# Performance work log

Measured on AMD Instinct MI355X. Metric: run time of the kernel, lower is better.

Reference implementation:

```python
import jax, jax.numpy as jnp
import numpy as np

ALPHA = 0.2  # leaky-relu negative slope
N_NODES = 50000
IN_F = 256
OUT_F = 64
N_EDGES = 1600000


def setup_inputs() -> dict:
    key = jax.random.key(0)
    k1, k2, k3, k4 = jax.random.split(key, 4)
    x = jax.random.normal(k1, (N_NODES, IN_F), dtype=jnp.float32)
    # xavier_normal-ish scales for params
    W = jax.random.normal(k2, (IN_F, OUT_F), dtype=jnp.float32) * (1.414 * (2.0 / (IN_F + OUT_F)) ** 0.5)
    a = jax.random.normal(k3, (1, 2 * OUT_F), dtype=jnp.float32) * (1.414 * (2.0 / (1 + 2 * OUT_F)) ** 0.5)
    edge_index = jax.random.randint(k4, (2, N_EDGES), 0, N_NODES, dtype=jnp.int64)
    return {"x": x, "W": W, "a": a, "edge_index": edge_index}


def reference(x, W, a, edge_index):
    N = x.shape[0]
    src = edge_index[0]  # row index of sparse adjacency (aggregation target)
    dst = edge_index[1]  # column index (neighbor being gathered)
    h = x @ W  # [N, out]
    out_f = h.shape[1]
    # a @ cat(h[src], h[dst]) == (h @ a1)[src] + (h @ a2)[dst]
    a1 = a[0, :out_f]
    a2 = a[0, out_f:]
    s_src = h @ a1  # [N]
    s_dst = h @ a2  # [N]
    score = s_src[src] + s_dst[dst]  # [E]
    edge_e = jnp.exp(-jax.nn.leaky_relu(score, negative_slope=ALPHA))  # [E]
    # e_rowsum[i] = sum_{e: src==i} edge_e[e]
    e_rowsum = jax.ops.segment_sum(edge_e, src, num_segments=N)  # [N]
    # h_prime[i] = sum_{e: src==i} edge_e[e] * h[dst[e]]
    h_prime = jax.ops.segment_sum(edge_e[:, None] * h[dst], src, num_segments=N)  # [N, out]
    h_prime = h_prime / e_rowsum[:, None]
    return jax.nn.elu(h_prime)
```

## Files before the change

kernel.cpp:

```cpp
#include <hip/hip_runtime.h>
#include <hip/hip_bf16.h>


#define ALPHA 0.2f
#define KDIM 256
#define FDIM 64

typedef __bf16 bf16x8 __attribute__((ext_vector_type(8)));
typedef float f32x4 __attribute__((ext_vector_type(4)));
typedef unsigned int u32;
typedef unsigned short u16;

#define BIN_CHUNK 8192
#define BUCKET_CAP 16384

__global__ __launch_bounds__(256) void gat_wt_kernel(
    const float* __restrict__ W, __hip_bfloat16* __restrict__ w_t)
{
    const int t = blockIdx.x * 256 + threadIdx.x;
    if (t < KDIM * FDIM) {
        const int k = t >> 6;
        const int n = t & 63;
        w_t[n * KDIM + k] = __float2bfloat16(W[t]);
    }
}

__global__ __launch_bounds__(256) void gat_gemm_kernel(
    const float* __restrict__ x, const __hip_bfloat16* __restrict__ w_tp,
    const float* __restrict__ a, __hip_bfloat16* __restrict__ h_bf,
    float* __restrict__ s_src, float* __restrict__ s_dst, int N)
{
    const int lane = threadIdx.x & 63;
    const int wv = threadIdx.x >> 6;
    const int m0 = blockIdx.x * 64 + wv * 16;
    const int c = lane & 15;
    const int q = lane >> 4;

    const int mrow = m0 + c;
    const float* xp = x + (long)(mrow < N ? mrow : N - 1) * KDIM;
    const __bf16* wt = (const __bf16*)w_tp;

    f32x4 acc[4];
#pragma unroll
    for (int ct = 0; ct < 4; ++ct) acc[ct] = (f32x4){0.f, 0.f, 0.f, 0.f};

#pragma unroll 2
    for (int kc = 0; kc < 8; ++kc) {
        const int k0 = kc * 32 + q * 8;
        const float4 xa = *(const float4*)(xp + k0);
        const float4 xb = *(const float4*)(xp + k0 + 4);
        bf16x8 af;
        af[0] = (__bf16)xa.x; af[1] = (__bf16)xa.y;
        af[2] = (__bf16)xa.z; af[3] = (__bf16)xa.w;
        af[4] = (__bf16)xb.x; af[5] = (__bf16)xb.y;
        af[6] = (__bf16)xb.z; af[7] = (__bf16)xb.w;
#pragma unroll
        for (int ct = 0; ct < 4; ++ct) {
            const bf16x8 bf = *(const bf16x8*)(wt + (ct * 16 + c) * KDIM + k0);
            acc[ct] = __builtin_amdgcn_mfma_f32_16x16x32_bf16(af, bf, acc[ct], 0, 0, 0);
        }
    }

    float a1c[4], a2c[4];
#pragma unroll
    for (int ct = 0; ct < 4; ++ct) {
        a1c[ct] = a[ct * 16 + c];
        a2c[ct] = a[FDIM + ct * 16 + c];
    }
    float s1r[4], s2r[4];
#pragma unroll
    for (int reg = 0; reg < 4; ++reg) {
        float s1 = 0.f, s2 = 0.f;
#pragma unroll
        for (int ct = 0; ct < 4; ++ct) {
            s1 += acc[ct][reg] * a1c[ct];
            s2 += acc[ct][reg] * a2c[ct];
        }
        s1r[reg] = s1; s2r[reg] = s2;
    }
#pragma unroll
    for (int off = 1; off < 16; off <<= 1) {
#pragma unroll
        for (int reg = 0; reg < 4; ++reg) {
            s1r[reg] += __shfl_xor(s1r[reg], off);
            s2r[reg] += __shfl_xor(s2r[reg], off);
        }
    }

#pragma unroll
    for (int reg = 0; reg < 4; ++reg) {
        const int row = m0 + q * 4 + reg;
        if (row < N) {
#pragma unroll
            for (int ct = 0; ct < 4; ++ct)
                h_bf[(long)row * FDIM + ct * 16 + c] = __float2bfloat16(acc[ct][reg]);
            if (c == 0) { s_src[row] = s1r[reg]; s_dst[row] = s2r[reg]; }
        }
    }
}

__global__ __launch_bounds__(256) void gat_bhist_kernel(
    const int* __restrict__ srcA, int* __restrict__ bcnt, int E, int NB)
{
    __shared__ int hist[256];
    const int t = threadIdx.x;
    hist[t] = 0;
    __syncthreads();
    const int base = blockIdx.x * BIN_CHUNK;
    const int cnt = min(BIN_CHUNK, E - base);
    for (int i = t; i < cnt; i += 256)
        atomicAdd(&hist[srcA[base + i] >> 8], 1);
    __syncthreads();
    if (t < NB && hist[t] > 0) atomicAdd(&bcnt[t], hist[t]);
}

__global__ __launch_bounds__(256) void gat_bscan_kernel(
    const int* __restrict__ bcnt, int* __restrict__ bbase,
    int* __restrict__ bcur, int NB)
{
    __shared__ int wsum[4];
    const int t = threadIdx.x;
    const int lane = t & 63;
    const int w = t >> 6;
    const int v = (t < NB) ? bcnt[t] : 0;
    int incl = v;
#pragma unroll
    for (int off = 1; off < 64; off <<= 1) {
        const int nv = __shfl_up(incl, off);
        if (lane >= off) incl += nv;
    }
    if (lane == 63) wsum[w] = incl;
    __syncthreads();
    int woff = 0;
    if (w > 0) woff += wsum[0];
    if (w > 1) woff += wsum[1];
    if (w > 2) woff += wsum[2];
    const int excl = woff + incl - v;
    bbase[t] = excl;
    if (t < NB) bcur[t] = excl;
    if (t == 0) bbase[256] = wsum[0] + wsum[1] + wsum[2] + wsum[3];
}

__global__ __launch_bounds__(256) void gat_bin_kernel(
    const int* __restrict__ srcA, const int* __restrict__ dstA,
    int* __restrict__ bcur, u32* __restrict__ pair, int E, int NB)
{
    __shared__ u32 chunk[BIN_CHUNK];
    __shared__ int hist[256];
    __shared__ int lcur[256];
    const int t = threadIdx.x;
    hist[t] = 0;
    __syncthreads();

    const int base = blockIdx.x * BIN_CHUNK;
    const int cnt = min(BIN_CHUNK, E - base);
    for (int i = t; i < cnt; i += 256) {
        const int s = srcA[base + i];
        const int d = dstA[base + i];
        chunk[i] = ((u32)(s >> 8) << 24) | ((u32)(s & 255) << 16) | (u32)d;
        atomicAdd(&hist[s >> 8], 1);
    }
    __syncthreads();
    if (t < NB) lcur[t] = (hist[t] > 0) ? atomicAdd(&bcur[t], hist[t]) : 0;
    __syncthreads();
    for (int i = t; i < cnt; i += 256) {
        const u32 p = chunk[i];
        const int b = p >> 24;
        const int pos = atomicAdd(&lcur[b], 1);
        pair[pos] = p & 0x00FFFFFFu;
    }
}

__global__ __launch_bounds__(256) void gat_bsort_kernel(
    const u32* __restrict__ pair, const int* __restrict__ bbase,
    int* __restrict__ offs, int* __restrict__ sorted_dst, int N, int NB)
{
    __shared__ u32 chunk[BUCKET_CAP];
    __shared__ u16 sorted_l[BUCKET_CAP];
    __shared__ int cur[256];
    __shared__ int wsum[4];

    const int b = blockIdx.x;
    const int t = threadIdx.x;
    const int lane = t & 63;
    const int w = t >> 6;
    const int s0 = b << 8;
    const int e0 = bbase[b];
    const int e1 = bbase[b + 1];
    const int n = min(e1 - e0, BUCKET_CAP);

    cur[t] = 0;
    __syncthreads();
    for (int i = t; i < n; i += 256) {
        const u32 p = pair[e0 + i];
        chunk[i] = p;
        atomicAdd(&cur[p >> 16], 1);
    }
    __syncthreads();
    const int v = cur[t];
    int incl = v;
#pragma unroll
    for (int off = 1; off < 64; off <<= 1) {
        const int nv = __shfl_up(incl, off);
        if (lane >= off) incl += nv;
    }
    if (lane == 63) wsum[w] = incl;
    __syncthreads();
    int woff = 0;
    if (w > 0) woff += wsum[0];
    if (w > 1) woff += wsum[1];
    if (w > 2) woff += wsum[2];
    const int excl = woff + incl - v;
    if (s0 + t < N) offs[s0 + t] = e0 + excl;
    if (b == NB - 1 && t == 0) offs[N] = e1;
    __syncthreads();
    cur[t] = excl;
    __syncthreads();
    for (int i = t; i < n; i += 256) {
        const u32 p = chunk[i];
        const int slot = atomicAdd(&cur[p >> 16], 1);
        sorted_l[slot] = (u16)(p & 0xFFFFu);
    }
    __syncthreads();
    for (int i = t; i < n; i += 256)
        sorted_dst[e0 + i] = (int)sorted_l[i];
}

__global__ __launch_bounds__(256) void gat_gather_kernel(
    const int* __restrict__ offs, const int* __restrict__ sorted_dst,
    const float* __restrict__ s_src, const float* __restrict__ s_dst,
    const __hip_bfloat16* __restrict__ h_bf, float* __restrict__ out, int N)
{
    const int node = blockIdx.x * 4 + (threadIdx.x >> 6);
    if (node >= N) return;
    const int lane = threadIdx.x & 63;
    const int q = lane >> 3;
    const int c = lane & 7;

    const int start = offs[node];
    const int end = offs[node + 1];
    const float ssrc = s_src[node];
    const __bf16* hb = (const __bf16*)h_bf;

    float acc[8];
#pragma unroll
    for (int j = 0; j < 8; ++j) acc[j] = 0.f;
    float wsum = 0.f;

    for (int e = start + q; e < end; e += 8) {
        const int d = sorted_dst[e];
        const float sc = ssrc + s_dst[d];
        const float lr = sc > 0.f ? sc : ALPHA * sc;
        const float wgt = __expf(-lr);
        const bf16x8 hv = *(const bf16x8*)(hb + (long)d * FDIM + 8 * c);
#pragma unroll
        for (int j = 0; j < 8; ++j) acc[j] += wgt * (float)hv[j];
        wsum += wgt;
    }

#pragma unroll
    for (int off = 8; off < 64; off <<= 1) {
#pragma unroll
        for (int j = 0; j < 8; ++j) acc[j] += __shfl_xor(acc[j], off);
        wsum += __shfl_xor(wsum, off);
    }

    if (q == 0) {
        const float inv = 1.0f / wsum;
        float o[8];
#pragma unroll
        for (int j = 0; j < 8; ++j) {
            const float v = acc[j] * inv;
            o[j] = v > 0.f ? v : expm1f(v);
        }
        float* op = &out[(long)node * FDIM + 8 * c];
        *(float4*)op = make_float4(o[0], o[1], o[2], o[3]);
        *(float4*)(op + 4) = make_float4(o[4], o[5], o[6], o[7]);
    }
}

extern "C" void kernel_launch(void* const* d_in, const int* in_sizes, int n_in,
                              void* d_out, int out_size, void* d_ws, size_t ws_size,
                              hipStream_t stream) {
    const float* x = (const float*)d_in[0];
    const float* W = (const float*)d_in[1];
    const float* a = (const float*)d_in[2];
    const int* ei  = (const int*)d_in[3];

    const int N = in_sizes[0] / KDIM;
    const int E = in_sizes[3] / 2;
    const int NB = (N + 255) >> 8;
    const int* srcA = ei;
    const int* dstA = ei + E;

    __hip_bfloat16* h_bf = (__hip_bfloat16*)d_ws;
    __hip_bfloat16* w_t  = h_bf + (size_t)N * FDIM;
    float* s_src = (float*)(w_t + KDIM * FDIM);
    float* s_dst = s_src + N;
    int* offs    = (int*)(s_dst + N);
    int* bcnt    = offs + N + 4;
    int* bbase   = bcnt + 256;
    int* bcur    = bbase + 260;
    u32* pair    = (u32*)(bcur + 256);
    int* sorted_dst = (int*)(pair + E);
    float* out   = (float*)d_out;

    hipMemsetAsync(bcnt, 0, 256 * sizeof(int), stream);

    gat_wt_kernel<<<dim3((KDIM * FDIM + 255) / 256), dim3(256), 0, stream>>>(W, w_t);
    gat_gemm_kernel<<<dim3((N + 63) / 64), dim3(256), 0, stream>>>(
        x, w_t, a, h_bf, s_src, s_dst, N);

    const int nchunks = (E + BIN_CHUNK - 1) / BIN_CHUNK;
    gat_bhist_kernel<<<dim3(nchunks), dim3(256), 0, stream>>>(srcA, bcnt, E, NB);
    gat_bscan_kernel<<<dim3(1), dim3(256), 0, stream>>>(bcnt, bbase, bcur, NB);
    gat_bin_kernel<<<dim3(nchunks), dim3(256), 0, stream>>>(srcA, dstA, bcur, pair, E, NB);
    gat_bsort_kernel<<<dim3(NB), dim3(256), 0, stream>>>(pair, bbase, offs, sorted_dst, N, NB);

    gat_gather_kernel<<<dim3((N + 3) / 4), dim3(256), 0, stream>>>(
        offs, sorted_dst, s_src, s_dst, h_bf, out, N);
}
```

Baseline: 205.0 us.

## Restructure edge binning into per-chunk local sort and precompute fp16 edge weights

Replaces the global histogram, scan and atomic binning pipeline with a per-chunk local counting sort that records per-chunk bucket offsets. A single-block kernel then derives bucket bases, and the bucket sort gathers its segments from every chunk. The bucket sort also computes each edge's attention weight and packs it as fp16 into the high half of the destination index, so the gather kernel no longer reads s_src/s_dst or evaluates exp. This removes the memset, one kernel and the global atomics. In exchange, every bucket block walks all chunk offset tables, weights lose precision in fp16, and the 16-bit dst packing assumes N < 65536.

```diff
diff --git a/kernel.cpp b/kernel.cpp
--- a/kernel.cpp
+++ b/kernel.cpp
@@ -1,18 +1,19 @@
 #include <hip/hip_runtime.h>
 #include <hip/hip_bf16.h>
+#include <hip/hip_fp16.h>
 
 
 #define ALPHA 0.2f
 #define KDIM 256
 #define FDIM 64
+#define BIN_CHUNK 8192
+#define BUCKET_CAP 16384
+#define OFFW 257
 
 typedef __bf16 bf16x8 __attribute__((ext_vector_type(8)));
 typedef float f32x4 __attribute__((ext_vector_type(4)));
 typedef unsigned int u32;
 typedef unsigned short u16;
-
-#define BIN_CHUNK 8192
-#define BUCKET_CAP 16384
 
 __global__ __launch_bounds__(256) void gat_wt_kernel(
     const float* __restrict__ W, __hip_bfloat16* __restrict__ w_t)
@@ -99,30 +100,25 @@
     }
 }
 
-__global__ __launch_bounds__(256) void gat_bhist_kernel(
-    const int* __restrict__ srcA, int* __restrict__ bcnt, int E, int NB)
+__global__ __launch_bounds__(256) void gat_bin_kernel(
+    const int* __restrict__ srcA, const int* __restrict__ dstA,
+    int* __restrict__ off_blk, u32* __restrict__ pair, int E)
 {
     __shared__ int hist[256];
-    const int t = threadIdx.x;
-    hist[t] = 0;
-    __syncthreads();
-    const int base = blockIdx.x * BIN_CHUNK;
-    const int cnt = min(BIN_CHUNK, E - base);
-    for (int i = t; i < cnt; i += 256)
-        atomicAdd(&hist[srcA[base + i] >> 8], 1);
-    __syncthreads();
-    if (t < NB && hist[t] > 0) atomicAdd(&bcnt[t], hist[t]);
-}
-
-__global__ __launch_bounds__(256) void gat_bscan_kernel(
-    const int* __restrict__ bcnt, int* __restrict__ bbase,
-    int* __restrict__ bcur, int NB)
-{
+    __shared__ int cur[256];
     __shared__ int wsum[4];
     const int t = threadIdx.x;
     const int lane = t & 63;
     const int w = t >> 6;
-    const int v = (t < NB) ? bcnt[t] : 0;
+    const int base = blockIdx.x * BIN_CHUNK;
+    const int cnt = min(BIN_CHUNK, E - base);
+
+    hist[t] = 0;
+    __syncthreads();
+    for (int i = t; i < cnt; i += 256) atomicAdd(&hist[srcA[base + i] >> 8], 1);
+    __syncthreads();
+
+    const int v = hist[t];
     int incl = v;
 #pragma unroll
     for (int off = 1; off < 64; off <<= 1) {
@@ -136,67 +132,85 @@
     if (w > 1) woff += wsum[1];
     if (w > 2) woff += wsum[2];
     const int excl = woff + incl - v;
-    bbase[t] = excl;
-    if (t < NB) bcur[t] = excl;
-    if (t == 0) bbase[256] = wsum[0] + wsum[1] + wsum[2] + wsum[3];
-}
-
-__global__ __launch_bounds__(256) void gat_bin_kernel(
-    const int* __restrict__ srcA, const int* __restrict__ dstA,
-    int* __restrict__ bcur, u32* __restrict__ pair, int E, int NB)
-{
-    __shared__ u32 chunk[BIN_CHUNK];
-    __shared__ int hist[256];
-    __shared__ int lcur[256];
-    const int t = threadIdx.x;
-    hist[t] = 0;
-    __syncthreads();
-
-    const int base = blockIdx.x * BIN_CHUNK;
-    const int cnt = min(BIN_CHUNK, E - base);
+    off_blk[blockIdx.x * OFFW + t] = excl;
+    if (t == 0) off_blk[blockIdx.x * OFFW + 256] = cnt;
+    cur[t] = excl;
+    __syncthreads();
+
     for (int i = t; i < cnt; i += 256) {
         const int s = srcA[base + i];
         const int d = dstA[base + i];
-        chunk[i] = ((u32)(s >> 8) << 24) | ((u32)(s & 255) << 16) | (u32)d;
-        atomicAdd(&hist[s >> 8], 1);
-    }
-    __syncthreads();
-    if (t < NB) lcur[t] = (hist[t] > 0) ? atomicAdd(&bcur[t], hist[t]) : 0;
-    __syncthreads();
-    for (int i = t; i < cnt; i += 256) {
-        const u32 p = chunk[i];
-        const int b = p >> 24;
-        const int pos = atomicAdd(&lcur[b], 1);
-        pair[pos] = p & 0x00FFFFFFu;
-    }
+        const int pos = atomicAdd(&cur[s >> 8], 1);
+        pair[base + pos] = ((u32)(s & 255) << 16) | (u32)d;
+    }
+}
+
+__global__ __launch_bounds__(256) void gat_bbase_kernel(
+    const int* __restrict__ off_blk, int* __restrict__ bbase, int NBLK)
+{
+    __shared__ int wsum[4];
+    const int t = threadIdx.x;
+    const int lane = t & 63;
+    const int w = t >> 6;
+    int total = 0;
+    for (int blk = 0; blk < NBLK; ++blk) {
+        const int* ob = off_blk + blk * OFFW;
+        total += ob[t + 1] - ob[t];
+    }
+    int incl = total;
+#pragma unroll
+    for (int off = 1; off < 64; off <<= 1) {
+        const int nv = __shfl_up(incl, off);
+        if (lane >= off) incl += nv;
+    }
+    if (lane == 63) wsum[w] = incl;
+    __syncthreads();
+    int woff = 0;
+    if (w > 0) woff += wsum[0];
+    if (w > 1) woff += wsum[1];
+    if (w > 2) woff += wsum[2];
+    const int excl = woff + incl - total;
+    bbase[t] = excl;
+    if (t == 255) bbase[256] = excl + total;
 }
 
 __global__ __launch_bounds__(256) void gat_bsort_kernel(
-    const u32* __restrict__ pair, const int* __restrict__ bbase,
-    int* __restrict__ offs, int* __restrict__ sorted_dst, int N, int NB)
+    const u32* __restrict__ pair, const int* __restrict__ off_blk,
+    const int* __restrict__ bbase, const float* __restrict__ s_src,
+    const float* __restrict__ s_dst, int* __restrict__ offs,
+    u32* __restrict__ sorted_pk, int N, int NBLK, int NB)
 {
     __shared__ u32 chunk[BUCKET_CAP];
-    __shared__ u16 sorted_l[BUCKET_CAP];
     __shared__ int cur[256];
+    __shared__ float ssl[256];
     __shared__ int wsum[4];
 
     const int b = blockIdx.x;
     const int t = threadIdx.x;
     const int lane = t & 63;
     const int w = t >> 6;
-    const int s0 = b << 8;
     const int e0 = bbase[b];
     const int e1 = bbase[b + 1];
     const int n = min(e1 - e0, BUCKET_CAP);
 
+    int pos = 0;
+    for (int blk = 0; blk < NBLK; ++blk) {
+        const int s = off_blk[blk * OFFW + b];
+        const int c = off_blk[blk * OFFW + b + 1] - s;
+        const u32* pp = pair + blk * BIN_CHUNK + s;
+        for (int i = t; i < c; i += 256) {
+            const int dp = pos + i;
+            if (dp < BUCKET_CAP) chunk[dp] = pp[i];
+        }
+        pos += c;
+    }
     cur[t] = 0;
-    __syncthreads();
-    for (int i = t; i < n; i += 256) {
-        const u32 p = pair[e0 + i];
-        chunk[i] = p;
-        atomicAdd(&cur[p >> 16], 1);
-    }
-    __syncthreads();
+    ssl[t] = (b * 256 + t < N) ? s_src[b * 256 + t] : 0.f;
+    __syncthreads();
+
+    for (int i = t; i < n; i += 256) atomicAdd(&cur[chunk[i] >> 16], 1);
+    __syncthreads();
+
     const int v = cur[t];
     int incl = v;
 #pragma unroll
@@ -211,24 +225,27 @@
     if (w > 1) woff += wsum[1];
     if (w > 2) woff += wsum[2];
     const int excl = woff + incl - v;
-    if (s0 + t < N) offs[s0 + t] = e0 + excl;
+    if (b * 256 + t < N) offs[b * 256 + t] = e0 + excl;
     if (b == NB - 1 && t == 0) offs[N] = e1;
     __syncthreads();
     cur[t] = excl;
     __syncthreads();
+
     for (int i = t; i < n; i += 256) {
         const u32 p = chunk[i];
-        const int slot = atomicAdd(&cur[p >> 16], 1);
-        sorted_l[slot] = (u16)(p & 0xFFFFu);
-    }
-    __syncthreads();
-    for (int i = t; i < n; i += 256)
-        sorted_dst[e0 + i] = (int)sorted_l[i];
+        const int sl = p >> 16;
+        const int d = (int)(p & 0xFFFFu);
+        const int slot = atomicAdd(&cur[sl], 1);
+        const float sc = ssl[sl] + s_dst[d];
+        const float lr = sc > 0.f ? sc : ALPHA * sc;
+        const float wgt = __expf(-lr);
+        const u32 wh = (u32)__half_as_ushort(__float2half(wgt));
+        sorted_pk[e0 + slot] = (u32)d | (wh << 16);
+    }
 }
 
 __global__ __launch_bounds__(256) void gat_gather_kernel(
-    const int* __restrict__ offs, const int* __restrict__ sorted_dst,
-    const float* __restrict__ s_src, const float* __restrict__ s_dst,
+    const int* __restrict__ offs, const u32* __restrict__ sorted_pk,
     const __hip_bfloat16* __restrict__ h_bf, float* __restrict__ out, int N)
 {
     const int node = blockIdx.x * 4 + (threadIdx.x >> 6);
@@ -239,7 +256,6 @@
 
     const int start = offs[node];
     const int end = offs[node + 1];
-    const float ssrc = s_src[node];
     const __bf16* hb = (const __bf16*)h_bf;
 
     float acc[8];
@@ -247,11 +263,11 @@
     for (int j = 0; j < 8; ++j) acc[j] = 0.f;
     float wsum = 0.f;
 
+#pragma unroll 2
     for (int e = start + q; e < end; e += 8) {
-        const int d = sorted_dst[e];
-        const float sc = ssrc + s_dst[d];
-        const float lr = sc > 0.f ? sc : ALPHA * sc;
-        const float wgt = __expf(-lr);
+        const u32 p = sorted_pk[e];
+        const float wgt = __half2float(__ushort_as_half((u16)(p >> 16)));
+        const int d = (int)(p & 0xFFFFu);
         const bf16x8 hv = *(const bf16x8*)(hb + (long)d * FDIM + 8 * c);
 #pragma unroll
         for (int j = 0; j < 8; ++j) acc[j] += wgt * (float)hv[j];
@@ -290,6 +306,7 @@
     const int N = in_sizes[0] / KDIM;
     const int E = in_sizes[3] / 2;
     const int NB = (N + 255) >> 8;
+    const int NBLK = (E + BIN_CHUNK - 1) / BIN_CHUNK;
     const int* srcA = ei;
     const int* dstA = ei + E;
 
@@ -298,25 +315,21 @@
     float* s_src = (float*)(w_t + KDIM * FDIM);
     float* s_dst = s_src + N;
     int* offs    = (int*)(s_dst + N);
-    int* bcnt    = offs + N + 4;
-    int* bbase   = bcnt + 256;
-    int* bcur    = bbase + 260;
-    u32* pair    = (u32*)(bcur + 256);
-    int* sorted_dst = (int*)(pair + E);
+    int* off_blk = offs + N + 4;
+    int* bbase   = off_blk + NBLK * OFFW;
+    u32* pair    = (u32*)(bbase + 260);
+    u32* sorted_pk = pair + E;
     float* out   = (float*)d_out;
-
-    hipMemsetAsync(bcnt, 0, 256 * sizeof(int), stream);
 
     gat_wt_kernel<<<dim3((KDIM * FDIM + 255) / 256), dim3(256), 0, stream>>>(W, w_t);
     gat_gemm_kernel<<<dim3((N + 63) / 64), dim3(256), 0, stream>>>(
         x, w_t, a, h_bf, s_src, s_dst, N);
 
-    const int nchunks = (E + BIN_CHUNK - 1) / BIN_CHUNK;
-    gat_bhist_kernel<<<dim3(nchunks), dim3(256), 0, stream>>>(srcA, bcnt, E, NB);
-    gat_bscan_kernel<<<dim3(1), dim3(256), 0, stream>>>(bcnt, bbase, bcur, NB);
-    gat_bin_kernel<<<dim3(nchunks), dim3(256), 0, stream>>>(srcA, dstA, bcur, pair, E, NB);
-    gat_bsort_kernel<<<dim3(NB), dim3(256), 0, stream>>>(pair, bbase, offs, sorted_dst, N, NB);
+    gat_bin_kernel<<<dim3(NBLK), dim3(256), 0, stream>>>(srcA, dstA, off_blk, pair, E);
+    gat_bbase_kernel<<<dim3(1), dim3(256), 0, stream>>>(off_blk, bbase, NBLK);
+    gat_bsort_kernel<<<dim3(NB), dim3(256), 0, stream>>>(
+        pair, off_blk, bbase, s_src, s_dst, offs, sorted_pk, N, NBLK, NB);
 
     gat_gather_kernel<<<dim3((N + 3) / 4), dim3(256), 0, stream>>>(
-        offs, sorted_dst, s_src, s_dst, h_bf, out, N);
-}
+        offs, sorted_pk, h_bf, out, N);
+}
```

Result: slower. 293.0 us (+42.9%).

## Use finer 64-node buckets and precompute fp16 edge weights during bucket sort

Applied to the files above, without the earlier changes.

Buckets shrink from 256 to 64 source nodes, which gives 782 sort blocks and smaller shared arrays. The bin kernel now re-reads src/dst instead of staging them in shared memory. The sort kernel computes each edge's attention weight and packs it as fp16 with the 16-bit dst index, so the gather no longer does the random s_dst lookup or the exp. This adds fp16 rounding of the weights, relies on dst fitting in 16 bits and bucket counts fitting BUCKET_CAP, and adds an unroll hint to the gather loop.

```diff
diff --git a/kernel.cpp b/kernel.cpp
--- a/kernel.cpp
+++ b/kernel.cpp
@@ -1,18 +1,18 @@
 #include <hip/hip_runtime.h>
 #include <hip/hip_bf16.h>
+#include <hip/hip_fp16.h>
 
 
 #define ALPHA 0.2f
 #define KDIM 256
 #define FDIM 64
+#define BIN_CHUNK 8192
+#define BUCKET_CAP 4096
 
 typedef __bf16 bf16x8 __attribute__((ext_vector_type(8)));
 typedef float f32x4 __attribute__((ext_vector_type(4)));
 typedef unsigned int u32;
 typedef unsigned short u16;
-
-#define BIN_CHUNK 8192
-#define BUCKET_CAP 16384
 
 __global__ __launch_bounds__(256) void gat_wt_kernel(
     const float* __restrict__ W, __hip_bfloat16* __restrict__ w_t)
@@ -100,30 +100,33 @@
 }
 
 __global__ __launch_bounds__(256) void gat_bhist_kernel(
-    const int* __restrict__ srcA, int* __restrict__ bcnt, int E, int NB)
-{
-    __shared__ int hist[256];
+    const int* __restrict__ srcA, int* __restrict__ bcnt, int E, int NBU)
+{
+    __shared__ int hist[1024];
     const int t = threadIdx.x;
-    hist[t] = 0;
+    for (int j = t; j < 1024; j += 256) hist[j] = 0;
     __syncthreads();
     const int base = blockIdx.x * BIN_CHUNK;
     const int cnt = min(BIN_CHUNK, E - base);
     for (int i = t; i < cnt; i += 256)
-        atomicAdd(&hist[srcA[base + i] >> 8], 1);
-    __syncthreads();
-    if (t < NB && hist[t] > 0) atomicAdd(&bcnt[t], hist[t]);
+        atomicAdd(&hist[srcA[base + i] >> 6], 1);
+    __syncthreads();
+    for (int j = t; j < NBU; j += 256) {
+        const int v = hist[j];
+        if (v) atomicAdd(&bcnt[j], v);
+    }
 }
 
 __global__ __launch_bounds__(256) void gat_bscan_kernel(
-    const int* __restrict__ bcnt, int* __restrict__ bbase,
-    int* __restrict__ bcur, int NB)
+    const int* __restrict__ bcnt, int* __restrict__ bbase, int* __restrict__ bcur)
 {
     __shared__ int wsum[4];
     const int t = threadIdx.x;
     const int lane = t & 63;
     const int w = t >> 6;
-    const int v = (t < NB) ? bcnt[t] : 0;
-    int incl = v;
+    const int4 v = *(const int4*)&bcnt[4 * t];
+    const int tsum = v.x + v.y + v.z + v.w;
+    int incl = tsum;
 #pragma unroll
     for (int off = 1; off < 64; off <<= 1) {
         const int nv = __shfl_up(incl, off);
@@ -135,61 +138,60 @@
     if (w > 0) woff += wsum[0];
     if (w > 1) woff += wsum[1];
     if (w > 2) woff += wsum[2];
-    const int excl = woff + incl - v;
-    bbase[t] = excl;
-    if (t < NB) bcur[t] = excl;
-    if (t == 0) bbase[256] = wsum[0] + wsum[1] + wsum[2] + wsum[3];
+    const int e0 = woff + incl - tsum;
+    const int4 o = make_int4(e0, e0 + v.x, e0 + v.x + v.y, e0 + v.x + v.y + v.z);
+    *(int4*)&bbase[4 * t] = o;
+    *(int4*)&bcur[4 * t] = o;
+    if (t == 255) bbase[1024] = e0 + tsum;
 }
 
 __global__ __launch_bounds__(256) void gat_bin_kernel(
     const int* __restrict__ srcA, const int* __restrict__ dstA,
-    int* __restrict__ bcur, u32* __restrict__ pair, int E, int NB)
-{
-    __shared__ u32 chunk[BIN_CHUNK];
-    __shared__ int hist[256];
-    __shared__ int lcur[256];
+    int* __restrict__ bcur, u32* __restrict__ pair, int E, int NBU)
+{
+    __shared__ int hist[1024];
+    __shared__ int lcur[1024];
     const int t = threadIdx.x;
-    hist[t] = 0;
-    __syncthreads();
-
+    for (int j = t; j < 1024; j += 256) hist[j] = 0;
+    __syncthreads();
     const int base = blockIdx.x * BIN_CHUNK;
     const int cnt = min(BIN_CHUNK, E - base);
+    for (int i = t; i < cnt; i += 256)
+        atomicAdd(&hist[srcA[base + i] >> 6], 1);
+    __syncthreads();
+    for (int j = t; j < NBU; j += 256) {
+        const int v = hist[j];
+        lcur[j] = v ? atomicAdd(&bcur[j], v) : 0;
+    }
+    __syncthreads();
     for (int i = t; i < cnt; i += 256) {
         const int s = srcA[base + i];
         const int d = dstA[base + i];
-        chunk[i] = ((u32)(s >> 8) << 24) | ((u32)(s & 255) << 16) | (u32)d;
-        atomicAdd(&hist[s >> 8], 1);
-    }
-    __syncthreads();
-    if (t < NB) lcur[t] = (hist[t] > 0) ? atomicAdd(&bcur[t], hist[t]) : 0;
-    __syncthreads();
-    for (int i = t; i < cnt; i += 256) {
-        const u32 p = chunk[i];
-        const int b = p >> 24;
-        const int pos = atomicAdd(&lcur[b], 1);
-        pair[pos] = p & 0x00FFFFFFu;
+        const int pos = atomicAdd(&lcur[s >> 6], 1);
+        pair[pos] = ((u32)(s & 63) << 16) | (u32)d;
     }
 }
 
 __global__ __launch_bounds__(256) void gat_bsort_kernel(
     const u32* __restrict__ pair, const int* __restrict__ bbase,
-    int* __restrict__ offs, int* __restrict__ sorted_dst, int N, int NB)
+    const float* __restrict__ s_src, const float* __restrict__ s_dst,
+    int* __restrict__ offs, u32* __restrict__ sorted_pk, int N, int NBU)
 {
     __shared__ u32 chunk[BUCKET_CAP];
-    __shared__ u16 sorted_l[BUCKET_CAP];
-    __shared__ int cur[256];
-    __shared__ int wsum[4];
+    __shared__ int cur[64];
+    __shared__ float ssl[64];
 
     const int b = blockIdx.x;
     const int t = threadIdx.x;
-    const int lane = t & 63;
-    const int w = t >> 6;
-    const int s0 = b << 8;
+    const int s0 = b << 6;
     const int e0 = bbase[b];
     const int e1 = bbase[b + 1];
     const int n = min(e1 - e0, BUCKET_CAP);
 
-    cur[t] = 0;
+    if (t < 64) {
+        cur[t] = 0;
+        ssl[t] = (s0 + t < N) ? s_src[s0 + t] : 0.f;
+    }
     __syncthreads();
     for (int i = t; i < n; i += 256) {
         const u32 p = pair[e0 + i];
@@ -197,38 +199,35 @@
         atomicAdd(&cur[p >> 16], 1);
     }
     __syncthreads();
-    const int v = cur[t];
-    int incl = v;
-#pragma unroll
-    for (int off = 1; off < 64; off <<= 1) {
-        const int nv = __shfl_up(incl, off);
-        if (lane >= off) incl += nv;
-    }
-    if (lane == 63) wsum[w] = incl;
-    __syncthreads();
-    int woff = 0;
-    if (w > 0) woff += wsum[0];
-    if (w > 1) woff += wsum[1];
-    if (w > 2) woff += wsum[2];
-    const int excl = woff + incl - v;
-    if (s0 + t < N) offs[s0 + t] = e0 + excl;
-    if (b == NB - 1 && t == 0) offs[N] = e1;
-    __syncthreads();
-    cur[t] = excl;
+    if (t < 64) {
+        const int v = cur[t];
+        int incl = v;
+#pragma unroll
+        for (int off = 1; off < 64; off <<= 1) {
+            const int nv = __shfl_up(incl, off);
+            if (t >= off) incl += nv;
+        }
+        const int excl = incl - v;
+        if (s0 + t < N) offs[s0 + t] = e0 + excl;
+        cur[t] = excl;
+    }
+    if (b == NBU - 1 && t == 0) offs[N] = e1;
     __syncthreads();
     for (int i = t; i < n; i += 256) {
         const u32 p = chunk[i];
-        const int slot = atomicAdd(&cur[p >> 16], 1);
-        sorted_l[slot] = (u16)(p & 0xFFFFu);
-    }
-    __syncthreads();
-    for (int i = t; i < n; i += 256)
-        sorted_dst[e0 + i] = (int)sorted_l[i];
+        const int sl = p >> 16;
+        const int d = (int)(p & 0xFFFFu);
+        const int slot = atomicAdd(&cur[sl], 1);
+        const float sc = ssl[sl] + s_dst[d];
+        const float lr = sc > 0.f ? sc : ALPHA * sc;
+        const float wgt = __expf(-lr);
+        const u32 wh = (u32)__half_as_ushort(__float2half(wgt));
+        sorted_pk[e0 + slot] = (u32)d | (wh << 16);
+    }
 }
 
 __global__ __launch_bounds__(256) void gat_gather_kernel(
-    const int* __restrict__ offs, const int* __restrict__ sorted_dst,
-    const float* __restrict__ s_src, const float* __restrict__ s_dst,
+    const int* __restrict__ offs, const u32* __restrict__ sorted_pk,
     const __hip_bfloat16* __restrict__ h_bf, float* __restrict__ out, int N)
 {
     const int node = blockIdx.x * 4 + (threadIdx.x >> 6);
@@ -239,7 +238,6 @@
 
     const int start = offs[node];
     const int end = offs[node + 1];
-    const float ssrc = s_src[node];
     const __bf16* hb = (const __bf16*)h_bf;
 
     float acc[8];
@@ -247,11 +245,11 @@
     for (int j = 0; j < 8; ++j) acc[j] = 0.f;
     float wsum = 0.f;
 
+#pragma unroll 2
     for (int e = start + q; e < end; e += 8) {
-        const int d = sorted_dst[e];
-        const float sc = ssrc + s_dst[d];
-        const float lr = sc > 0.f ? sc : ALPHA * sc;
-        const float wgt = __expf(-lr);
+        const u32 p = sorted_pk[e];
+        const float wgt = __half2float(__ushort_as_half((u16)(p >> 16)));
+        const int d = (int)(p & 0xFFFFu);
         const bf16x8 hv = *(const bf16x8*)(hb + (long)d * FDIM + 8 * c);
 #pragma unroll
         for (int j = 0; j < 8; ++j) acc[j] += wgt * (float)hv[j];
@@ -289,7 +287,8 @@
 
     const int N = in_sizes[0] / KDIM;
     const int E = in_sizes[3] / 2;
-    const int NB = (N + 255) >> 8;
+    const int NBU = (N + 63) >> 6;
+    const int NBLK = (E + BIN_CHUNK - 1) / BIN_CHUNK;
     const int* srcA = ei;
     const int* dstA = ei + E;
 
@@ -299,24 +298,24 @@
     float* s_dst = s_src + N;
     int* offs    = (int*)(s_dst + N);
     int* bcnt    = offs + N + 4;
-    int* bbase   = bcnt + 256;
-    int* bcur    = bbase + 260;
-    u32* pair    = (u32*)(bcur + 256);
-    int* sorted_dst = (int*)(pair + E);
+    int* bbase   = bcnt + 1024;
+    int* bcur    = bbase + 1028;
+    u32* pair    = (u32*)(bcur + 1024);
+    u32* sorted_pk = pair + E;
     float* out   = (float*)d_out;
 
-    hipMemsetAsync(bcnt, 0, 256 * sizeof(int), stream);
+    hipMemsetAsync(bcnt, 0, 1024 * sizeof(int), stream);
 
     gat_wt_kernel<<<dim3((KDIM * FDIM + 255) / 256), dim3(256), 0, stream>>>(W, w_t);
     gat_gemm_kernel<<<dim3((N + 63) / 64), dim3(256), 0, stream>>>(
         x, w_t, a, h_bf, s_src, s_dst, N);
 
-    const int nchunks = (E + BIN_CHUNK - 1) / BIN_CHUNK;
-    gat_bhist_kernel<<<dim3(nchunks), dim3(256), 0, stream>>>(srcA, bcnt, E, NB);
-    gat_bscan_kernel<<<dim3(1), dim3(256), 0, stream>>>(bcnt, bbase, bcur, NB);
-    gat_bin_kernel<<<dim3(nchunks), dim3(256), 0, stream>>>(srcA, dstA, bcur, pair, E, NB);
-    gat_bsort_kernel<<<dim3(NB), dim3(256), 0, stream>>>(pair, bbase, offs, sorted_dst, N, NB);
+    gat_bhist_kernel<<<dim3(NBLK), dim3(256), 0, stream>>>(srcA, bcnt, E, NBU);
+    gat_bscan_kernel<<<dim3(1), dim3(256), 0, stream>>>(bcnt, bbase, bcur);
+    gat_bin_kernel<<<dim3(NBLK), dim3(256), 0, stream>>>(srcA, dstA, bcur, pair, E, NBU);
+    gat_bsort_kernel<<<dim3(NBU), dim3(256), 0, stream>>>(
+        pair, bbase, s_src, s_dst, offs, sorted_pk, N, NBU);
 
     gat_gather_kernel<<<dim3((N + 3) / 4), dim3(256), 0, stream>>>(
-        offs, sorted_dst, s_src, s_dst, h_bf, out, N);
-}
+        offs, sorted_pk, h_bf, out, N);
+}
```

Measured after the change: 210.8 us. 2.8% more time.
